# Optimization experiments

Hardware: AMD Instinct MI355X
Metric: run time of the kernel (lower is better)

Reference implementation:

```python
import jax, jax.numpy as jnp
import numpy as np


def _project_to_unitary_2x2(W):
    # Polar projection of batched 2x2 real matrices via SVD: U @ Vh.
    U, _, Vh = jnp.linalg.svd(W, full_matrices=False)
    return U @ Vh


def setup_inputs() -> dict:
    key = jax.random.key(0)
    k1, k2, k3 = jax.random.split(key, 3)
    B, T, C = 8, 4096, 2048
    G = C // 2
    x = jax.random.normal(k1, (B, T, C), dtype=jnp.float32)
    # Torch init: eye(2) + 0.01*randn per pair
    W_pairs = jnp.eye(2, dtype=jnp.float32)[None] + 0.01 * jax.random.normal(k2, (G, 2, 2), dtype=jnp.float32)
    phase = jax.random.normal(k3, (G,), dtype=jnp.float32)
    return {"x": x, "W_pairs": W_pairs, "phase": phase}


def reference(x, W_pairs, phase):
    B, T, C = x.shape
    G = C // 2
    # Project per-pair 2x2 to nearest orthonormal matrix (unitary_project=True)
    W = _project_to_unitary_2x2(W_pairs)  # [G,2,2]
    # Phase rotation matrices R(phi): [[c,-s],[s,c]]
    c, s = jnp.cos(phase), jnp.sin(phase)
    R = jnp.stack([jnp.stack([c, -s], -1), jnp.stack([s, c], -1)], -2)  # [G,2,2]
    # Compose rotation * unitary once, then apply as a single pass on [B,T,G,2]
    M = jnp.einsum('gij,gjk->gik', R, W)  # [G,2,2]
    xg = x.reshape(B, T, G, 2)
    y = jnp.einsum('gij,btgj->btgi', M, xg)
    return y.reshape(B, T, C)
```

## Files before the change

### kernel.cpp

```cpp
#include <hip/hip_runtime.h>

__global__ void bsu_compute_M(const float* __restrict__ W,
                              const float* __restrict__ phase,
                              float4* __restrict__ M, int G) {
    int g = blockIdx.x * blockDim.x + threadIdx.x;
    if (g >= G) return;
    float a = W[4 * g + 0];
    float b = W[4 * g + 1];
    float c = W[4 * g + 2];
    float d = W[4 * g + 3];
    float det = a * d - b * c;
    float q00, q01, q10, q11;
    if (det >= 0.0f) {
        float p = a + d;
        float q = b - c;
        float inv = rsqrtf(p * p + q * q);
        q00 = p * inv;  q01 = q * inv;
        q10 = -q * inv; q11 = p * inv;
    } else {
        float p = a - d;
        float q = b + c;
        float inv = rsqrtf(p * p + q * q);
        q00 = p * inv; q01 = q * inv;
        q10 = q * inv; q11 = -p * inv;
    }
    float cs, sn;
    __sincosf(phase[g], &sn, &cs);
    float4 m;
    m.x = cs * q00 - sn * q10;
    m.y = cs * q01 - sn * q11;
    m.z = sn * q00 + cs * q10;
    m.w = sn * q01 + cs * q11;
    M[g] = m;
}

__global__ __launch_bounds__(256) void bsu_apply(const float4* __restrict__ x,
                                                 const float4* __restrict__ M,
                                                 float4* __restrict__ y,
                                                 int n4, int gmask) {
    int i = blockIdx.x * blockDim.x + threadIdx.x;
    int stride = gridDim.x * blockDim.x;
    for (; i < n4; i += stride) {
        float4 v = x[i];
        int g0 = (2 * i) & gmask;
        float4 m0 = M[g0];
        float4 m1 = M[g0 + 1];
        float4 o;
        o.x = m0.x * v.x + m0.y * v.y;
        o.y = m0.z * v.x + m0.w * v.y;
        o.z = m1.x * v.z + m1.y * v.w;
        o.w = m1.z * v.z + m1.w * v.w;
        y[i] = o;
    }
}

extern "C" void kernel_launch(void* const* d_in, const int* in_sizes, int n_in,
                              void* d_out, int out_size, void* d_ws, size_t ws_size,
                              hipStream_t stream) {
    const float* x     = (const float*)d_in[0];
    const float* Wp    = (const float*)d_in[1];
    const float* phase = (const float*)d_in[2];
    float* y = (float*)d_out;

    int G = in_sizes[2];
    int n = in_sizes[0];
    int n4 = n / 4;

    float4* M = (float4*)d_ws;

    bsu_compute_M<<<(G + 255) / 256, 256, 0, stream>>>(Wp, phase, M, G);

    int blocks = (n4 + 255) / 256;
    if (blocks > 2048) blocks = 2048;
    bsu_apply<<<blocks, 256, 0, stream>>>((const float4*)x, M, (float4*)y,
                                          n4, G - 1);
}
```

Measured before the change: 110.6 us.

## Fuse matrix computation into apply kernel with per-thread register-resident coefficients

Removes the separate kernel that builds the per-pair 2x2 matrices. Each thread of the streaming kernel now computes its own two matrices once and keeps them in registers. This relies on the grid stride being a multiple of the row width, so a thread always sees the same channel pair; when it is not, the launch falls back to one element per thread. Loads and stores of x and y also become nontemporal, which avoids polluting the cache on this pure streaming pass. The gains are one fewer launch and no per-iteration reads of the matrices, at the cost of redundant sincos and rsqrt work across threads.

```diff
diff --git a/kernel.cpp b/kernel.cpp
--- a/kernel.cpp
+++ b/kernel.cpp
@@ -1,56 +1,57 @@
 #include <hip/hip_runtime.h>
 
-__global__ void bsu_compute_M(const float* __restrict__ W,
-                              const float* __restrict__ phase,
-                              float4* __restrict__ M, int G) {
-    int g = blockIdx.x * blockDim.x + threadIdx.x;
-    if (g >= G) return;
-    float a = W[4 * g + 0];
-    float b = W[4 * g + 1];
-    float c = W[4 * g + 2];
-    float d = W[4 * g + 3];
+typedef float f32x4 __attribute__((ext_vector_type(4)));
+
+__device__ __forceinline__ void compute_M(const float4* __restrict__ W,
+                                          const float* __restrict__ phase,
+                                          int g,
+                                          float& m00, float& m01,
+                                          float& m10, float& m11) {
+    float4 w = W[g];
+    float a = w.x, b = w.y, c = w.z, d = w.w;
     float det = a * d - b * c;
     float q00, q01, q10, q11;
     if (det >= 0.0f) {
-        float p = a + d;
-        float q = b - c;
+        float p = a + d, q = b - c;
         float inv = rsqrtf(p * p + q * q);
         q00 = p * inv;  q01 = q * inv;
         q10 = -q * inv; q11 = p * inv;
     } else {
-        float p = a - d;
-        float q = b + c;
+        float p = a - d, q = b + c;
         float inv = rsqrtf(p * p + q * q);
         q00 = p * inv; q01 = q * inv;
         q10 = q * inv; q11 = -p * inv;
     }
     float cs, sn;
     __sincosf(phase[g], &sn, &cs);
-    float4 m;
-    m.x = cs * q00 - sn * q10;
-    m.y = cs * q01 - sn * q11;
-    m.z = sn * q00 + cs * q10;
-    m.w = sn * q01 + cs * q11;
-    M[g] = m;
+    m00 = cs * q00 - sn * q10;
+    m01 = cs * q01 - sn * q11;
+    m10 = sn * q00 + cs * q10;
+    m11 = sn * q01 + cs * q11;
 }
 
-__global__ __launch_bounds__(256) void bsu_apply(const float4* __restrict__ x,
-                                                 const float4* __restrict__ M,
-                                                 float4* __restrict__ y,
+__global__ __launch_bounds__(256) void bsu_fused(const f32x4* __restrict__ x,
+                                                 const float4* __restrict__ W,
+                                                 const float* __restrict__ phase,
+                                                 f32x4* __restrict__ y,
                                                  int n4, int gmask) {
-    int i = blockIdx.x * blockDim.x + threadIdx.x;
-    int stride = gridDim.x * blockDim.x;
-    for (; i < n4; i += stride) {
-        float4 v = x[i];
-        int g0 = (2 * i) & gmask;
-        float4 m0 = M[g0];
-        float4 m1 = M[g0 + 1];
-        float4 o;
-        o.x = m0.x * v.x + m0.y * v.y;
-        o.y = m0.z * v.x + m0.w * v.y;
-        o.z = m1.x * v.z + m1.y * v.w;
-        o.w = m1.z * v.z + m1.w * v.w;
-        y[i] = o;
+    int i0 = blockIdx.x * 256 + threadIdx.x;
+    int stride = gridDim.x * 256;
+    int g0 = (2 * i0) & gmask;
+
+    float a00, a01, a10, a11;
+    float b00, b01, b10, b11;
+    compute_M(W, phase, g0,     a00, a01, a10, a11);
+    compute_M(W, phase, g0 + 1, b00, b01, b10, b11);
+
+    for (int i = i0; i < n4; i += stride) {
+        f32x4 v = __builtin_nontemporal_load(&x[i]);
+        f32x4 o;
+        o.x = a00 * v.x + a01 * v.y;
+        o.y = a10 * v.x + a11 * v.y;
+        o.z = b00 * v.z + b01 * v.w;
+        o.w = b10 * v.z + b11 * v.w;
+        __builtin_nontemporal_store(o, &y[i]);
     }
 }
 
@@ -66,12 +67,10 @@
     int n = in_sizes[0];
     int n4 = n / 4;
 
-    float4* M = (float4*)d_ws;
+    int blocks = 2048;
+    int row4 = G / 2;
+    if ((blocks * 256) % row4 != 0) blocks = (n4 + 255) / 256;
 
-    bsu_compute_M<<<(G + 255) / 256, 256, 0, stream>>>(Wp, phase, M, G);
-
-    int blocks = (n4 + 255) / 256;
-    if (blocks > 2048) blocks = 2048;
-    bsu_apply<<<blocks, 256, 0, stream>>>((const float4*)x, M, (float4*)y,
-                                          n4, G - 1);
+    bsu_fused<<<blocks, 256, 0, stream>>>((const f32x4*)x, (const float4*)Wp,
+                                          phase, (f32x4*)y, n4, G - 1);
 }
```

After: 99.71 us. 9.9% less time.
